# Performance work log

Measured on AMD Instinct MI355X. Metric: run time of the kernel, lower is better.

Reference implementation:

```python
import jax, jax.numpy as jnp
import numpy as np

B, N, C, H = 64, 300, 256, 8  # batch, patches (img 1x300, patch 1x1), dim, heads
STD = 0.02


def setup_inputs() -> dict:
    key = jax.random.key(0)
    ks = jax.random.split(key, 6)
    return {
        "x": jax.random.normal(ks[0], (B, N, C), jnp.float32),
        "Wqk": jax.random.normal(ks[1], (2 * C, C), jnp.float32) * STD,
        "Wv": jax.random.normal(ks[2], (C, C), jnp.float32) * STD,
        "Wpos": jax.random.normal(ks[3], (H, 3), jnp.float32) * STD,
        "bpos": jnp.zeros((H,), jnp.float32),
        "Wproj": jax.random.normal(ks[4], (C, C), jnp.float32) * STD,
        "bproj": jnp.zeros((C,), jnp.float32),
        "gating": jnp.ones((H,), jnp.float32),
    }


def _rel_indices(n):
    d = (jnp.arange(n)[None, :] - jnp.arange(n)[:, None]).astype(jnp.float32)
    return jnp.stack([d, jnp.zeros_like(d), d * d], axis=-1)  # [N, N, 3]


def reference(x, Wqk, Wv, Wpos, bpos, Wproj, bproj, gating):
    Bb, Nn, Cc = x.shape
    Hh = gating.shape[0]
    hd = Cc // Hh
    scale = hd ** -0.5

    qk = (x @ Wqk.T).reshape(Bb, Nn, 2, Hh, hd)
    q = qk[:, :, 0].transpose(0, 2, 1, 3)  # [B,H,N,hd]
    k = qk[:, :, 1].transpose(0, 2, 1, 3)

    patch_score = jax.nn.softmax(jnp.einsum('bhnd,bhmd->bhnm', q, k) * scale, axis=-1)

    rel = _rel_indices(Nn)                               # [N,N,3]
    pos_score = (rel @ Wpos.T + bpos).transpose(2, 0, 1)  # [H,N,N]
    pos_score = jax.nn.softmax(pos_score, axis=-1)

    g = jax.nn.sigmoid(gating)[None, :, None, None]       # [1,H,1,1]
    attn = (1.0 - g) * patch_score + g * pos_score[None]
    attn = attn / attn.sum(axis=-1, keepdims=True)

    v = (x @ Wv.T).reshape(Bb, Nn, Hh, hd).transpose(0, 2, 1, 3)  # [B,H,N,hd]
    out = jnp.einsum('bhnm,bhmd->bhnd', attn, v)
    out = out.transpose(0, 2, 1, 3).reshape(Bb, Nn, Cc)
    return out @ Wproj.T + bproj
```

## Files before the change

kernel.cpp:

```cpp
#include <hip/hip_runtime.h>


#define NSEQ 300
#define HEADS 8
#define HD 32

typedef short v8s __attribute__((ext_vector_type(8)));
typedef float v4f __attribute__((ext_vector_type(4)));
typedef unsigned int v4u __attribute__((ext_vector_type(4)));

__device__ __forceinline__ ushort f2bf(float f) {
    unsigned u = __float_as_uint(f);
    u = (u + 0x7FFFu + ((u >> 16) & 1u)) >> 16;
    return (ushort)u;
}

__device__ __forceinline__ unsigned pk2bf(float a, float b) {
    unsigned ua = __float_as_uint(a), ub = __float_as_uint(b);
    ua += 0x7FFFu + ((ua >> 16) & 1u);
    ub += 0x7FFFu + ((ub >> 16) & 1u);
    return __builtin_amdgcn_perm(ub, ua, 0x07060302);
}

__device__ __forceinline__ unsigned cvtpk(float a, float b) {
    unsigned r;
    asm("v_cvt_pk_bf16_f32 %0, %1, %2" : "=v"(r) : "v"(a), "v"(b));
    return r;
}

__device__ __forceinline__ float fexp2(float x) {
    float r; asm("v_exp_f32 %0, %1" : "=v"(r) : "v"(x)); return r;
}

__device__ __forceinline__ void gl_lds16(const ushort* g, ushort* l) {
    __builtin_amdgcn_global_load_lds(
        (const __attribute__((address_space(1))) void*)g,
        (__attribute__((address_space(3))) void*)l, 16, 0, 0);
}

__global__ __launch_bounds__(256) void prep_kernel(
    const float* __restrict__ x,
    const float* __restrict__ Wqk, const float* __restrict__ Wv,
    const float* __restrict__ Wproj, const float* __restrict__ Wpos,
    const float* __restrict__ bpos, const float* __restrict__ gating,
    ushort* __restrict__ x_bf, ushort* __restrict__ Wf,
    ushort* __restrict__ wproj_t, ushort* __restrict__ gpos)
{
    int bid = blockIdx.x, tid = threadIdx.x;
    if (bid < 2432) {
        int idx = bid * 256 + tid;
        int c8 = idx & 31;
        int mrow = idx >> 5;
        unsigned b = (unsigned)mrow / 304u;
        int r = mrow - (int)b * 304;
        v4u pk = {0u, 0u, 0u, 0u};
        if (r < 300) {
            const float* src = x + ((size_t)b * 300 + r) * 256 + c8 * 8;
            float4 f0 = *(const float4*)src;
            float4 f1 = *(const float4*)(src + 4);
            pk = (v4u){pk2bf(f0.x, f0.y), pk2bf(f0.z, f0.w),
                       pk2bf(f1.x, f1.y), pk2bf(f1.z, f1.w)};
        }
        *(v4u*)&x_bf[(size_t)mrow * 256 + c8 * 8] = pk;
        return;
    }
    if (bid < 3040) {
        int sub = bid - 2432;
        int h = sub / 76;
        int i = (sub % 76) * 4 + (tid >> 6);
        int lane = tid & 63;
        ushort* gr = gpos + ((size_t)h * 304 + i) * 304;
        if (i >= NSEQ) {
#pragma unroll
            for (int t = 0; t < 5; ++t) {
                int j = lane + 64 * t;
                if (j < 304) gr[j] = 0;
            }
            return;
        }
        float w0 = Wpos[h * 3 + 0], w2 = Wpos[h * 3 + 2], bb = bpos[h];
        float g = 1.f / (1.f + __expf(-gating[h]));
        float sv[5]; float m2 = -1e30f;
#pragma unroll
        for (int t = 0; t < 5; ++t) {
            int j = lane + 64 * t;
            float d = (float)(j - i);
            float lg = fmaf(w2, d * d, fmaf(w0, d, bb));
            sv[t] = (j < NSEQ) ? lg : -1e30f;
            m2 = fmaxf(m2, sv[t]);
        }
#pragma unroll
        for (int off = 32; off > 0; off >>= 1) m2 = fmaxf(m2, __shfl_xor(m2, off));
        float sum = 0.f;
#pragma unroll
        for (int t = 0; t < 5; ++t) { sv[t] = __expf(sv[t] - m2); sum += sv[t]; }
#pragma unroll
        for (int off = 32; off > 0; off >>= 1) sum += __shfl_xor(sum, off);
        float gi = g / sum;
#pragma unroll
        for (int t = 0; t < 5; ++t) {
            int j = lane + 64 * t;
            if (j < NSEQ) gr[j] = f2bf(sv[t] * gi);
            else if (j < 304) gr[j] = 0;
        }
        return;
    }
    if (bid < 3136) {
        int idx = (bid - 3040) * 256 + tid;
        int c = idx & 7;
        int t = idx >> 3;
        int hk = t / 96;
        int wc = t - hk * 96;
        int h = hk >> 2, kt = hk & 3;
        const float* src;
        if (wc < 32)      src = Wqk + (size_t)(h * 32 + wc) * 256;
        else if (wc < 64) src = Wqk + (size_t)(256 + h * 32 + (wc - 32)) * 256;
        else              src = Wv + (size_t)(h * 32 + (wc - 64)) * 256;
        src += kt * 64 + c * 8;
        float4 f0 = *(const float4*)src;
        float4 f1 = *(const float4*)(src + 4);
        v4u pk = {pk2bf(f0.x, f0.y), pk2bf(f0.z, f0.w),
                  pk2bf(f1.x, f1.y), pk2bf(f1.z, f1.w)};
        *(v4u*)&Wf[((size_t)(hk * 96 + wc)) * 64 + ((c ^ (wc & 7)) * 8)] = pk;
        return;
    }
    {
        int idx = (bid - 3136) * 256 + tid;
        int m = idx >> 5, ck = idx & 31;
        const float* src = Wproj + (size_t)m * 256 + ck * 8;
        int rt = m >> 7, rr = m & 127, kt = ck >> 3, c = ck & 7;
        float4 f0 = *(const float4*)src;
        float4 f1 = *(const float4*)(src + 4);
        v4u pk = {pk2bf(f0.x, f0.y), pk2bf(f0.z, f0.w),
                  pk2bf(f1.x, f1.y), pk2bf(f1.z, f1.w)};
        *(v4u*)&wproj_t[((size_t)(rt * 4 + kt) * 128 + rr) * 64 + ((c ^ (rr & 7)) * 8)] = pk;
    }
}

__global__ __launch_bounds__(512, 4) void fused_qkv_attn(
    const ushort* __restrict__ x_bf, const ushort* __restrict__ Wf,
    const ushort* __restrict__ gpos, const float* __restrict__ gating,
    ushort* __restrict__ ot)
{
    __shared__ ushort smem[25600];
    ushort* Xs = smem;
    ushort* Wsh = smem + 19456;
    ushort* Ks = smem;
    ushort* Vt = smem + 12160;

    int bid = blockIdx.x, b = bid & 63, h = bid >> 6;
    int tid = threadIdx.x, wave = tid >> 6, lane = tid & 63, li = lane & 15, qd = lane >> 4;

    const ushort* xbb = x_bf + (size_t)b * 304 * 256;
    const ushort* wfh = Wf + (size_t)h * 4 * 6144;

    v4f acc[3][6];
#pragma unroll
    for (int i = 0; i < 3; ++i)
#pragma unroll
        for (int j = 0; j < 6; ++j) acc[i][j] = (v4f){0.f, 0.f, 0.f, 0.f};

    for (int kt = 0; kt < 4; ++kt) {
        gl_lds16(wfh + (size_t)kt * 6144 + tid * 8, Wsh + tid * 8);
        if (tid < 256)
            gl_lds16(wfh + (size_t)kt * 6144 + (512 + tid) * 8, Wsh + (512 + tid) * 8);
#pragma unroll
        for (int s = 0; s < 4; ++s) {
            int cch = s * 512 + tid;
            int r = cch >> 3, sl = cch & 7;
            gl_lds16(xbb + (size_t)r * 256 + kt * 64 + ((sl ^ (r & 7)) * 8),
                     Xs + cch * 8);
        }
        if (tid < 384) {
            int cch = 2048 + tid;
            int r = cch >> 3, sl = cch & 7;
            gl_lds16(xbb + (size_t)r * 256 + kt * 64 + ((sl ^ (r & 7)) * 8),
                     Xs + cch * 8);
        }
        __syncthreads();
#pragma unroll
        for (int kc = 0; kc < 64; kc += 32) {
            int cb = (kc >> 3) + qd;
            int cs = cb ^ (li & 7);
            v8s bw[6];
#pragma unroll
            for (int ct = 0; ct < 6; ++ct)
                bw[ct] = *(const v8s*)&Wsh[(ct * 16 + li) * 64 + cs * 8];
#pragma unroll
            for (int i = 0; i < 3; ++i) {
                int rt = wave + i * 8;
                if (rt < 19) {
                    v8s ax = *(const v8s*)&Xs[(rt * 16 + li) * 64 + cs * 8];
#pragma unroll
                    for (int ct = 0; ct < 6; ++ct)
                        acc[i][ct] = __builtin_amdgcn_mfma_f32_16x16x32_bf16(bw[ct], ax, acc[i][ct], 0, 0, 0);
                }
            }
        }
        __syncthreads();
    }

    const float QSC = 0.25503486063f;
    v4u q0 = {0,0,0,0}, q1 = {0,0,0,0}, q2 = {0,0,0,0};
    int srcA = ((qd & 1) << 5) + li;
    int srcB = srcA + 16;
#pragma unroll
    for (int i = 0; i < 3; ++i) {
        int rt = wave + i * 8;
        if (rt < 19) {
            unsigned W00 = cvtpk(acc[i][0][0] * QSC, acc[i][0][1] * QSC);
            unsigned W01 = cvtpk(acc[i][0][2] * QSC, acc[i][0][3] * QSC);
            unsigned W10 = cvtpk(acc[i][1][0] * QSC, acc[i][1][1] * QSC);
            unsigned W11 = cvtpk(acc[i][1][2] * QSC, acc[i][1][3] * QSC);
            unsigned a0 = __shfl(W00, srcA), a1 = __shfl(W01, srcA);
            unsigned a2 = __shfl(W00, srcB), a3 = __shfl(W01, srcB);
            unsigned b0 = __shfl(W10, srcA), b1 = __shfl(W11, srcA);
            unsigned b2 = __shfl(W10, srcB), b3 = __shfl(W11, srcB);
            bool hi = (qd >= 2);
            v4u qq = {hi ? b0 : a0, hi ? b1 : a1, hi ? b2 : a2, hi ? b3 : a3};
            if (i == 0) q0 = qq; else if (i == 1) q1 = qq; else q2 = qq;

            int row = rt * 16 + li;
#pragma unroll
            for (int ct = 2; ct < 4; ++ct) {
                uint2 wk = {cvtpk(acc[i][ct][0], acc[i][ct][1]),
                            cvtpk(acc[i][ct][2], acc[i][ct][3])};
                *(uint2*)&Ks[row * 40 + (ct - 2) * 16 + qd * 4] = wk;
            }
#pragma unroll
            for (int ct = 4; ct < 6; ++ct)
#pragma unroll
                for (int r = 0; r < 4; ++r)
                    Vt[((ct - 4) * 16 + qd * 4 + r) * 328 + row] = f2bf(acc[i][ct][r]);
        }
    }
    float g = 1.f / (1.f + __expf(-gating[h]));
    float omg = 1.f - g;
    __syncthreads();

    const ushort* ksp0 = &Ks[li * 40 + qd * 8];
    const ushort* vtp0 = &Vt[li * 328 + qd * 4];
    const ushort* vtp1 = &Vt[(16 + li) * 328 + qd * 4];
    const v4f z4 = {0.f, 0.f, 0.f, 0.f};

#pragma unroll 1
    for (int rg = wave; rg < 19; rg += 8) {
        int i0 = rg * 16;
        v8s bq = __builtin_bit_cast(v8s, q0);
        const ushort* gp = gpos + ((size_t)h * 304 + (i0 + li)) * 304 + qd * 4;

        v4f Oe0 = z4, Oe1 = z4, Og0 = z4, Og1 = z4;
        float esum = 0.f;

        v8s ak0 = *(const v8s*)(ksp0);
        v8s ak1 = *(const v8s*)(ksp0 + 640);
        uint2 v0a = *(const uint2*)(vtp0);
        uint2 v0b = *(const uint2*)(vtp0 + 16);
        uint2 v1a = *(const uint2*)(vtp1);
        uint2 v1b = *(const uint2*)(vtp1 + 16);
        uint2 gc0 = *(const uint2*)(gp);
        uint2 gc1 = *(const uint2*)(gp + 16);
        uint2 gn0 = *(const uint2*)(gp + 32);
        uint2 gn1 = *(const uint2*)(gp + 48);
        v4f s0n = __builtin_amdgcn_mfma_f32_16x16x32_bf16(ak0, bq, z4, 0, 0, 0);
        v4f s1n = __builtin_amdgcn_mfma_f32_16x16x32_bf16(ak1, bq, z4, 0, 0, 0);

#pragma unroll 1
        for (int p = 0; p < 9; ++p) {
            v4f s0 = s0n, s1 = s1n;
            v8s b0 = __builtin_bit_cast(v8s, (v4u){v0a.x, v0a.y, v0b.x, v0b.y});
            v8s b1 = __builtin_bit_cast(v8s, (v4u){v1a.x, v1a.y, v1b.x, v1b.y});
            v8s ag = __builtin_bit_cast(v8s, (v4u){gc0.x, gc0.y, gc1.x, gc1.y});
            gc0 = gn0; gc1 = gn1;
            int nt0 = 2 * p + 2;
            int nt1 = (p < 8) ? nt0 + 1 : 18;
            int gt0 = (p < 7) ? 2 * p + 4 : 18;
            int gt1 = (p < 7) ? 2 * p + 5 : 18;
            ak0 = *(const v8s*)(ksp0 + nt0 * 640);
            ak1 = *(const v8s*)(ksp0 + nt1 * 640);
            v0a = *(const uint2*)(vtp0 + nt0 * 16);
            v0b = *(const uint2*)(vtp0 + nt1 * 16);
            v1a = *(const uint2*)(vtp1 + nt0 * 16);
            v1b = *(const uint2*)(vtp1 + nt1 * 16);
            gn0 = *(const uint2*)(gp + gt0 * 16);
            gn1 = *(const uint2*)(gp + gt1 * 16);
            s0n = __builtin_amdgcn_mfma_f32_16x16x32_bf16(ak0, bq, z4, 0, 0, 0);
            s1n = __builtin_amdgcn_mfma_f32_16x16x32_bf16(ak1, bq, z4, 0, 0, 0);

            float e0 = fexp2(s0[0]);
            float e1 = fexp2(s0[1]);
            float e2 = fexp2(s0[2]);
            float e3 = fexp2(s0[3]);
            float f0 = fexp2(s1[0]);
            float f1 = fexp2(s1[1]);
            float f2 = fexp2(s1[2]);
            float f3 = fexp2(s1[3]);
            esum += ((e0 + e1) + (e2 + e3)) + ((f0 + f1) + (f2 + f3));
            v8s ae = __builtin_bit_cast(v8s, (v4u){cvtpk(e0, e1), cvtpk(e2, e3),
                                                   cvtpk(f0, f1), cvtpk(f2, f3)});
            __builtin_amdgcn_s_setprio(1);
            Oe0 = __builtin_amdgcn_mfma_f32_16x16x32_bf16(ae, b0, Oe0, 0, 0, 0);
            Oe1 = __builtin_amdgcn_mfma_f32_16x16x32_bf16(ae, b1, Oe1, 0, 0, 0);
            Og0 = __builtin_amdgcn_mfma_f32_16x16x32_bf16(ag, b0, Og0, 0, 0, 0);
            Og1 = __builtin_amdgcn_mfma_f32_16x16x32_bf16(ag, b1, Og1, 0, 0, 0);
            __builtin_amdgcn_s_setprio(0);
        }
        {
            float e0 = fexp2(s0n[0]);
            float e1 = fexp2(s0n[1]);
            float e2 = fexp2(s0n[2]);
            float e3 = fexp2(s0n[3]);
            if (qd == 3) { e0 = e1 = e2 = e3 = 0.f; }
            esum += (e0 + e1) + (e2 + e3);
            v8s ae = __builtin_bit_cast(v8s, (v4u){cvtpk(e0, e1), cvtpk(e2, e3), 0u, 0u});
            v8s ag = __builtin_bit_cast(v8s, (v4u){gc0.x, gc0.y, 0u, 0u});
            v8s b0 = __builtin_bit_cast(v8s, (v4u){v0a.x, v0a.y, 0u, 0u});
            v8s b1 = __builtin_bit_cast(v8s, (v4u){v1a.x, v1a.y, 0u, 0u});
            Oe0 = __builtin_amdgcn_mfma_f32_16x16x32_bf16(ae, b0, Oe0, 0, 0, 0);
            Oe1 = __builtin_amdgcn_mfma_f32_16x16x32_bf16(ae, b1, Oe1, 0, 0, 0);
            Og0 = __builtin_amdgcn_mfma_f32_16x16x32_bf16(ag, b0, Og0, 0, 0, 0);
            Og1 = __builtin_amdgcn_mfma_f32_16x16x32_bf16(ag, b1, Og1, 0, 0, 0);
        }
        esum += __shfl_xor(esum, 16);
        esum += __shfl_xor(esum, 32);
        float ps = omg / esum;
        float psr[4];
#pragma unroll
        for (int r = 0; r < 4; ++r) psr[r] = __shfl(ps, qd * 4 + r);
#pragma unroll
        for (int r = 0; r < 4; ++r) {
            int row = i0 + qd * 4 + r;
            if (row < NSEQ) {
                int m = b * NSEQ + row;
                int rt = m >> 7, rr = m & 127;
                int c0 = (h & 1) * 4 + (li >> 3);
                int p2 = li & 7;
                size_t tb = ((size_t)(rt * 4 + (h >> 1)) * 128 + rr) * 64;
                ot[tb + ((c0 ^ (rr & 7)) * 8) + p2] = f2bf(fmaf(psr[r], Oe0[r], Og0[r]));
                ot[tb + (((c0 + 2) ^ (rr & 7)) * 8) + p2] = f2bf(fmaf(psr[r], Oe1[r], Og1[r]));
            }
        }
        q0 = q1; q1 = q2;
    }
}

__global__ __launch_bounds__(256, 4) void gemm_proj_mfma(
    const ushort* __restrict__ A, const ushort* __restrict__ Bw,
    const float* __restrict__ bias, float* __restrict__ out)
{
    __shared__ ushort As[64 * 64];
    __shared__ ushort Bs[128 * 64];
    int tid = threadIdx.x;
    int wave = tid >> 6, lane = tid & 63, li = lane & 15, qd = lane >> 4;
    int rh = wave >> 1, ch = wave & 1;
    int by = blockIdx.y;
    const ushort* gA = A + ((size_t)(by >> 1) * 4 * 128 + (by & 1) * 64) * 64;
    const ushort* gB = Bw + (size_t)blockIdx.x * 4 * 8192;

    v4f acc[2][4];
#pragma unroll
    for (int i = 0; i < 2; ++i)
#pragma unroll
        for (int j = 0; j < 4; ++j) acc[i][j] = (v4f){0.f, 0.f, 0.f, 0.f};

    for (int kt = 0; kt < 4; ++kt) {
#pragma unroll
        for (int s = 0; s < 2; ++s) {
            int cch = s * 256 + tid;
            gl_lds16(gA + (size_t)kt * 128 * 64 + cch * 8, As + cch * 8);
        }
#pragma unroll
        for (int s = 0; s < 4; ++s) {
            int cch = s * 256 + tid;
            gl_lds16(gB + (size_t)kt * 8192 + cch * 8, Bs + cch * 8);
        }
        __syncthreads();
#pragma unroll
        for (int kc = 0; kc < 64; kc += 32) {
            int cb = (kc >> 3) + qd;
            int cs = cb ^ (li & 7);
            v8s a[2], b[4];
#pragma unroll
            for (int mt = 0; mt < 2; ++mt)
                a[mt] = *(const v8s*)&As[(rh * 32 + mt * 16 + li) * 64 + cs * 8];
#pragma unroll
            for (int nt = 0; nt < 4; ++nt)
                b[nt] = *(const v8s*)&Bs[(ch * 64 + nt * 16 + li) * 64 + cs * 8];
#pragma unroll
            for (int mt = 0; mt < 2; ++mt)
#pragma unroll
                for (int nt = 0; nt < 4; ++nt)
                    acc[mt][nt] = __builtin_amdgcn_mfma_f32_16x16x32_bf16(b[nt], a[mt], acc[mt][nt], 0, 0, 0);
        }
        __syncthreads();
    }

#pragma unroll
    for (int mt = 0; mt < 2; ++mt) {
        int row = by * 64 + rh * 32 + mt * 16 + li;
#pragma unroll
        for (int nt = 0; nt < 4; ++nt) {
            int col = blockIdx.x * 128 + ch * 64 + nt * 16 + qd * 4;
            float4 bv = *(const float4*)&bias[col];
            float4 st = {acc[mt][nt][0] + bv.x, acc[mt][nt][1] + bv.y,
                         acc[mt][nt][2] + bv.z, acc[mt][nt][3] + bv.w};
            *(float4*)&out[(size_t)row * 256 + col] = st;
        }
    }
}

extern "C" void kernel_launch(void* const* d_in, const int* in_sizes, int n_in,
                              void* d_out, int out_size, void* d_ws, size_t ws_size,
                              hipStream_t stream) {
    const float* x      = (const float*)d_in[0];
    const float* Wqk    = (const float*)d_in[1];
    const float* Wv     = (const float*)d_in[2];
    const float* Wpos   = (const float*)d_in[3];
    const float* bpos   = (const float*)d_in[4];
    const float* Wproj  = (const float*)d_in[5];
    const float* bproj  = (const float*)d_in[6];
    const float* gating = (const float*)d_in[7];
    float* out = (float*)d_out;

    ushort* gpos     = (ushort*)d_ws;
    ushort* Wf       = gpos + 739328;
    ushort* wproj_t  = Wf + 196608;
    ushort* o_t      = wproj_t + 65536;
    ushort* x_bf     = o_t + 4915200;

    prep_kernel<<<3168, 256, 0, stream>>>(x, Wqk, Wv, Wproj, Wpos, bpos, gating,
                                          x_bf, Wf, wproj_t, gpos);
    fused_qkv_attn<<<512, 512, 0, stream>>>(x_bf, Wf, gpos, gating, o_t);
    gemm_proj_mfma<<<dim3(2, 300), 256, 0, stream>>>(o_t, wproj_t, bproj, out);
}
```

Before: 122.9 us.

## Load full per-head QKV weight into LDS once and read X directly from global

Changes the preprocessed weight layout to full 256-wide rows with a 32-way XOR swizzle, so each block loads its whole per-head QKV weight slice into LDS with a single barrier instead of once per K-tile. The X tiles are no longer staged through shared memory; each wave loads its A fragments straight from global memory. This removes three of the four barrier pairs and the staged X copies, and shrinks LDS use. In exchange it relies on cache hits for the global X reads, which are strided 16-byte accesses, and loses the latency hiding that async LDS staging provided.

```diff
diff --git a/kernel.cpp b/kernel.cpp
--- a/kernel.cpp
+++ b/kernel.cpp
@@ -107,21 +107,21 @@
     }
     if (bid < 3136) {
         int idx = (bid - 3040) * 256 + tid;
-        int c = idx & 7;
-        int t = idx >> 3;
-        int hk = t / 96;
-        int wc = t - hk * 96;
-        int h = hk >> 2, kt = hk & 3;
+        int s = idx & 31;
+        int t = idx >> 5;
+        int h = t / 96;
+        int wc = t - h * 96;
+        int lc = s ^ (wc & 31);
         const float* src;
         if (wc < 32)      src = Wqk + (size_t)(h * 32 + wc) * 256;
         else if (wc < 64) src = Wqk + (size_t)(256 + h * 32 + (wc - 32)) * 256;
         else              src = Wv + (size_t)(h * 32 + (wc - 64)) * 256;
-        src += kt * 64 + c * 8;
+        src += lc * 8;
         float4 f0 = *(const float4*)src;
         float4 f1 = *(const float4*)(src + 4);
         v4u pk = {pk2bf(f0.x, f0.y), pk2bf(f0.z, f0.w),
                   pk2bf(f1.x, f1.y), pk2bf(f1.z, f1.w)};
-        *(v4u*)&Wf[((size_t)(hk * 96 + wc)) * 64 + ((c ^ (wc & 7)) * 8)] = pk;
+        *(v4u*)&Wf[((size_t)(h * 96 + wc)) * 256 + s * 8] = pk;
         return;
     }
     {
@@ -142,9 +142,8 @@
     const ushort* __restrict__ gpos, const float* __restrict__ gating,
     ushort* __restrict__ ot)
 {
-    __shared__ ushort smem[25600];
-    ushort* Xs = smem;
-    ushort* Wsh = smem + 19456;
+    __shared__ ushort smem[24576];
+    ushort* Wsh = smem;
     ushort* Ks = smem;
     ushort* Vt = smem + 12160;
 
@@ -152,7 +151,7 @@
     int tid = threadIdx.x, wave = tid >> 6, lane = tid & 63, li = lane & 15, qd = lane >> 4;
 
     const ushort* xbb = x_bf + (size_t)b * 304 * 256;
-    const ushort* wfh = Wf + (size_t)h * 4 * 6144;
+    const ushort* wfh = Wf + (size_t)h * 96 * 256;
 
     v4f acc[3][6];
 #pragma unroll
@@ -160,45 +159,44 @@
 #pragma unroll
         for (int j = 0; j < 6; ++j) acc[i][j] = (v4f){0.f, 0.f, 0.f, 0.f};
 
+#pragma unroll
+    for (int s = 0; s < 6; ++s) {
+        int c = s * 512 + tid;
+        gl_lds16(wfh + c * 8, Wsh + c * 8);
+    }
+    __syncthreads();
+
+#pragma unroll
     for (int kt = 0; kt < 4; ++kt) {
-        gl_lds16(wfh + (size_t)kt * 6144 + tid * 8, Wsh + tid * 8);
-        if (tid < 256)
-            gl_lds16(wfh + (size_t)kt * 6144 + (512 + tid) * 8, Wsh + (512 + tid) * 8);
-#pragma unroll
-        for (int s = 0; s < 4; ++s) {
-            int cch = s * 512 + tid;
-            int r = cch >> 3, sl = cch & 7;
-            gl_lds16(xbb + (size_t)r * 256 + kt * 64 + ((sl ^ (r & 7)) * 8),
-                     Xs + cch * 8);
-        }
-        if (tid < 384) {
-            int cch = 2048 + tid;
-            int r = cch >> 3, sl = cch & 7;
-            gl_lds16(xbb + (size_t)r * 256 + kt * 64 + ((sl ^ (r & 7)) * 8),
-                     Xs + cch * 8);
-        }
-        __syncthreads();
-#pragma unroll
-        for (int kc = 0; kc < 64; kc += 32) {
-            int cb = (kc >> 3) + qd;
-            int cs = cb ^ (li & 7);
+#pragma unroll
+        for (int kc = 0; kc < 2; ++kc) {
+            int xoff = kt * 64 + kc * 32 + qd * 8;
+            v8s ax0 = *(const v8s*)(xbb + (size_t)(wave * 16 + li) * 256 + xoff);
+            v8s ax1 = *(const v8s*)(xbb + (size_t)((wave + 8) * 16 + li) * 256 + xoff);
+            v8s ax2;
+            if (wave < 3)
+                ax2 = *(const v8s*)(xbb + (size_t)((wave + 16) * 16 + li) * 256 + xoff);
+            int cb = kt * 8 + kc * 4 + qd;
             v8s bw[6];
 #pragma unroll
+            for (int ct = 0; ct < 6; ++ct) {
+                int row = ct * 16 + li;
+                bw[ct] = *(const v8s*)&Wsh[row * 256 + (cb ^ (row & 31)) * 8];
+            }
+#pragma unroll
             for (int ct = 0; ct < 6; ++ct)
-                bw[ct] = *(const v8s*)&Wsh[(ct * 16 + li) * 64 + cs * 8];
-#pragma unroll
-            for (int i = 0; i < 3; ++i) {
-                int rt = wave + i * 8;
-                if (rt < 19) {
-                    v8s ax = *(const v8s*)&Xs[(rt * 16 + li) * 64 + cs * 8];
-#pragma unroll
-                    for (int ct = 0; ct < 6; ++ct)
-                        acc[i][ct] = __builtin_amdgcn_mfma_f32_16x16x32_bf16(bw[ct], ax, acc[i][ct], 0, 0, 0);
-                }
+                acc[0][ct] = __builtin_amdgcn_mfma_f32_16x16x32_bf16(bw[ct], ax0, acc[0][ct], 0, 0, 0);
+#pragma unroll
+            for (int ct = 0; ct < 6; ++ct)
+                acc[1][ct] = __builtin_amdgcn_mfma_f32_16x16x32_bf16(bw[ct], ax1, acc[1][ct], 0, 0, 0);
+            if (wave < 3) {
+#pragma unroll
+                for (int ct = 0; ct < 6; ++ct)
+                    acc[2][ct] = __builtin_amdgcn_mfma_f32_16x16x32_bf16(bw[ct], ax2, acc[2][ct], 0, 0, 0);
             }
         }
-        __syncthreads();
-    }
+    }
+    __syncthreads();
 
     const float QSC = 0.25503486063f;
     v4u q0 = {0,0,0,0}, q1 = {0,0,0,0}, q2 = {0,0,0,0};
```

Measured after the change: 127.0 us. 1.03x slower.
